# Kernel tuning notes

Measured on AMD Instinct MI355X. Metric: run time of the kernel, lower is better.

Reference implementation:

```python
import jax, jax.numpy as jnp
import numpy as np

GROUP_SIZE = 128

def setup_inputs() -> dict:
    key = jax.random.key(0)
    k0, k1, k2, k3 = jax.random.split(key, 4)
    B, S, K, N = 4, 16, 8192, 28672
    G = GROUP_SIZE
    x = jax.random.normal(k0, (B, S, K), dtype=jnp.float16)
    # packed uint8 stored as int32 (2 int4 nibbles per byte along K)
    w_packed = jax.random.randint(k1, (K // 2, N), 0, 256, dtype=jnp.int32)
    # per-group positive scales, typical magnitude for int4 quant of fp16 weights
    scales = (jax.random.uniform(k2, (K // G, N), dtype=jnp.float32) * 0.02 + 1e-4).astype(jnp.float16)
    bias = (jax.random.normal(k3, (N,), dtype=jnp.float16) * 0.02).astype(jnp.float16)
    return {"x": x, "w_packed": w_packed, "scales": scales, "bias": bias}

def _dequant(w_packed, scales):
    # w_packed: [K//2, N] ints in [0,256); low nibble -> even k, high nibble -> odd k
    low = (w_packed & 15) - 8          # [K//2, N] int32 in [-8, 7]
    high = ((w_packed >> 4) & 15) - 8  # [K//2, N]
    Kh, N = w_packed.shape
    w_int = jnp.stack([low, high], axis=1).reshape(Kh * 2, N)  # interleave -> [K, N]
    s = jnp.repeat(scales, GROUP_SIZE, axis=0)                 # [K, N] fp16
    return w_int.astype(jnp.float16) * s                       # [K, N] fp16

def reference(x, w_packed, scales, bias):
    # x: [B, S, K] fp16 -> y: [B, S, N] fp16
    w = _dequant(w_packed, scales)                 # [K, N] fp16
    lead = x.shape[:-1]
    x2 = x.reshape(-1, x.shape[-1])                # [M, K]
    # fp32 accumulation, fp16 output (matches Triton kernel's tl.dot accumulator)
    y = jnp.dot(x2, w, preferred_element_type=jnp.float32).astype(jnp.float16)
    y = y + bias
    return y.reshape(*lead, -1)
```

## Files before the change

### kernel.cpp

```cpp
#include <hip/hip_runtime.h>


typedef short  short8  __attribute__((ext_vector_type(8)));
typedef float  float4v __attribute__((ext_vector_type(4)));
typedef int    int4v   __attribute__((ext_vector_type(4)));
typedef unsigned int uint4v __attribute__((ext_vector_type(4)));

constexpr int Kd = 8192;
constexpr int Nd = 28672;
constexpr int KSPLIT = 4;
constexpr int GPS = 16;
constexpr int LDS_STRIDE = 68;

__device__ __forceinline__ unsigned f32_to_bf16_rn(float f) {
    unsigned u = __builtin_bit_cast(unsigned, f);
    return (u + 0x7FFFu + ((u >> 16) & 1u)) >> 16;
}

__global__ __launch_bounds__(256)
void init_y_kernel(const float* __restrict__ bias, float* __restrict__ y) {
    const int gid = blockIdx.x * 256 + threadIdx.x;
    const int m  = gid / (Nd / 4);
    const int nq = gid % (Nd / 4);
    ((float4v*)y)[(long)m * (Nd / 4) + nq] = ((const float4v*)bias)[nq];
}

__global__ __launch_bounds__(256)
void cvt_x_kernel(const float* __restrict__ x, unsigned short* __restrict__ o) {
    const int i = (blockIdx.x * 256 + threadIdx.x) * 8;
    float4v a = *(const float4v*)(x + i);
    float4v b = *(const float4v*)(x + i + 4);
    union { unsigned short s[8]; short8 v; } r;
    #pragma unroll
    for (int j = 0; j < 4; ++j) {
        r.s[j]     = (unsigned short)f32_to_bf16_rn(a[j]);
        r.s[4 + j] = (unsigned short)f32_to_bf16_rn(b[j]);
    }
    *(short8*)(o + i) = r.v;
}

__global__ __launch_bounds__(256, 6)
void int4_main_kernel(const unsigned short* __restrict__ xb,
                      const int*            __restrict__ wp,
                      const float*          __restrict__ scales,
                      float*                __restrict__ y)
{
    __shared__ unsigned lds_w[64 * LDS_STRIDE];

    const int t    = threadIdx.x;
    const int lane = t & 63;
    const int wv   = t >> 6;
    const int q    = lane >> 4;
    const int c    = lane & 15;
    const int n0   = blockIdx.x * 64;
    const int kz   = blockIdx.y;

    const int sr = t >> 4, ss = t & 15;
    const int*   wp_b = wp + (long)(kz * 1024 + sr) * Nd + n0 + 4 * ss;
    const float* sc_b = scales + (long)(kz * GPS) * Nd + n0 + 4 * ss;

    const unsigned short* xb_b = xb + (long)c * Kd + kz * 2048 + q * 8;

    float4v acc[4] = {};

    for (int g = 0; g < GPS; ++g) {
        const float4v s4 = *(const float4v*)(sc_b + (long)g * Nd);
        const int* wg = wp_b + (long)g * 64 * Nd;
        #pragma unroll
        for (int i = 0; i < 4; ++i) {
            int4v v = *(const int4v*)(wg + (long)i * 16 * Nd);
            uint4v pk;
            #pragma unroll
            for (int j = 0; j < 4; ++j) {
                float lo = (float)((v[j] & 15) - 8) * s4[j];
                float hi = (float)(((v[j] >> 4) & 15) - 8) * s4[j];
                pk[j] = f32_to_bf16_rn(lo) | (f32_to_bf16_rn(hi) << 16);
            }
            *(uint4v*)&lds_w[(i * 16 + sr) * LDS_STRIDE + 4 * ss] = pk;
        }
        __syncthreads();

        const unsigned short* xg = xb_b + g * 128;
        #pragma unroll
        for (int it = 0; it < 4; ++it) {
            union { short8 h; unsigned u[4]; } bu;
            #pragma unroll
            for (int i = 0; i < 4; ++i)
                bu.u[i] = lds_w[(it * 16 + q * 4 + i) * LDS_STRIDE + wv * 16 + c];
            const short8 b = bu.h;

            const unsigned short* xk = xg + it * 32;
            #pragma unroll
            for (int mt = 0; mt < 4; ++mt) {
                short8 a = *(const short8*)(xk + (long)mt * 16 * Kd);
                acc[mt] = __builtin_amdgcn_mfma_f32_16x16x32_bf16(a, b, acc[mt], 0, 0, 0);
            }
        }
        __syncthreads();
    }

    const int nw = n0 + wv * 16 + c;
    #pragma unroll
    for (int mt = 0; mt < 4; ++mt)
        #pragma unroll
        for (int r = 0; r < 4; ++r)
            atomicAdd(&y[(long)(mt * 16 + q * 4 + r) * Nd + nw], acc[mt][r]);
}

__global__ __launch_bounds__(256, 6)
void int4_main_nows_kernel(const float* __restrict__ xf,
                           const int*   __restrict__ wp,
                           const float* __restrict__ scales,
                           float*       __restrict__ y)
{
    __shared__ unsigned lds_w[64 * LDS_STRIDE];
    const int t = threadIdx.x, lane = t & 63, wv = t >> 6;
    const int q = lane >> 4, c = lane & 15;
    const int n0 = blockIdx.x * 64, kz = blockIdx.y;
    const int sr = t >> 4, ss = t & 15;
    const int*   wp_b = wp + (long)(kz * 1024 + sr) * Nd + n0 + 4 * ss;
    const float* sc_b = scales + (long)(kz * GPS) * Nd + n0 + 4 * ss;
    const float* xf_b = xf + (long)c * Kd + kz * 2048 + q * 8;
    float4v acc[4] = {};

    for (int g = 0; g < GPS; ++g) {
        const float4v s4 = *(const float4v*)(sc_b + (long)g * Nd);
        const int* wg = wp_b + (long)g * 64 * Nd;
        #pragma unroll
        for (int i = 0; i < 4; ++i) {
            int4v v = *(const int4v*)(wg + (long)i * 16 * Nd);
            uint4v pk;
            #pragma unroll
            for (int j = 0; j < 4; ++j) {
                float lo = (float)((v[j] & 15) - 8) * s4[j];
                float hi = (float)(((v[j] >> 4) & 15) - 8) * s4[j];
                pk[j] = f32_to_bf16_rn(lo) | (f32_to_bf16_rn(hi) << 16);
            }
            *(uint4v*)&lds_w[(i * 16 + sr) * LDS_STRIDE + 4 * ss] = pk;
        }
        __syncthreads();
        const float* xg = xf_b + g * 128;
        #pragma unroll
        for (int it = 0; it < 4; ++it) {
            union { short8 h; unsigned u[4]; } bu;
            #pragma unroll
            for (int i = 0; i < 4; ++i)
                bu.u[i] = lds_w[(it * 16 + q * 4 + i) * LDS_STRIDE + wv * 16 + c];
            const short8 b = bu.h;
            const float* xk = xg + it * 32;
            #pragma unroll
            for (int mt = 0; mt < 4; ++mt) {
                float4v a0 = *(const float4v*)(xk + (long)mt * 16 * Kd);
                float4v a1 = *(const float4v*)(xk + (long)mt * 16 * Kd + 4);
                union { unsigned short s[8]; short8 v; } r;
                #pragma unroll
                for (int j = 0; j < 4; ++j) {
                    r.s[j]     = (unsigned short)f32_to_bf16_rn(a0[j]);
                    r.s[4 + j] = (unsigned short)f32_to_bf16_rn(a1[j]);
                }
                acc[mt] = __builtin_amdgcn_mfma_f32_16x16x32_bf16(r.v, b, acc[mt], 0, 0, 0);
            }
        }
        __syncthreads();
    }
    const int nw = n0 + wv * 16 + c;
    #pragma unroll
    for (int mt = 0; mt < 4; ++mt)
        #pragma unroll
        for (int r = 0; r < 4; ++r)
            atomicAdd(&y[(long)(mt * 16 + q * 4 + r) * Nd + nw], acc[mt][r]);
}

extern "C" void kernel_launch(void* const* d_in, const int* in_sizes, int n_in,
                              void* d_out, int out_size, void* d_ws, size_t ws_size,
                              hipStream_t stream) {
    const float* x      = (const float*)d_in[0];
    const int*   wp     = (const int*)d_in[1];
    const float* scales = (const float*)d_in[2];
    const float* bias   = (const float*)d_in[3];
    float*       y      = (float*)d_out;

    init_y_kernel<<<dim3(1792), dim3(256), 0, stream>>>(bias, y);

    const size_t xb_bytes = (size_t)64 * Kd * sizeof(unsigned short);
    dim3 grid(Nd / 64, KSPLIT);
    dim3 block(256);

    if (ws_size >= xb_bytes) {
        unsigned short* xb = (unsigned short*)d_ws;
        cvt_x_kernel<<<dim3(256), dim3(256), 0, stream>>>(x, xb);
        int4_main_kernel<<<grid, block, 0, stream>>>(xb, wp, scales, y);
    } else {
        int4_main_nows_kernel<<<grid, block, 0, stream>>>(x, wp, scales, y);
    }
}
```

Before: 767.8 us.

## Double-buffer LDS and prefetch next weight group into registers

The main kernel now prefetches the next group's packed weights and scales into registers while the current group is dequantized and multiplied. It double-buffers the LDS tile so the trailing barrier can be dropped, and hoists all activation loads for the group ahead of the MFMA loop. Occupancy is lowered from 6 to 4 blocks per SM to leave room for the extra registers. The goal is to hide global-memory latency on the weight stream, at the cost of higher register pressure and fewer resident waves.

```diff
diff --git a/kernel.cpp b/kernel.cpp
--- a/kernel.cpp
+++ b/kernel.cpp
@@ -15,6 +15,10 @@
 __device__ __forceinline__ unsigned f32_to_bf16_rn(float f) {
     unsigned u = __builtin_bit_cast(unsigned, f);
     return (u + 0x7FFFu + ((u >> 16) & 1u)) >> 16;
+}
+
+__device__ __forceinline__ void sync_lds() {
+    asm volatile("s_waitcnt lgkmcnt(0)\n\ts_barrier" ::: "memory");
 }
 
 __global__ __launch_bounds__(256)
@@ -39,13 +43,13 @@
     *(short8*)(o + i) = r.v;
 }
 
-__global__ __launch_bounds__(256, 6)
+__global__ __launch_bounds__(256, 4)
 void int4_main_kernel(const unsigned short* __restrict__ xb,
                       const int*            __restrict__ wp,
                       const float*          __restrict__ scales,
                       float*                __restrict__ y)
 {
-    __shared__ unsigned lds_w[64 * LDS_STRIDE];
+    __shared__ unsigned lds_w[2 * 64 * LDS_STRIDE];
 
     const int t    = threadIdx.x;
     const int lane = t & 63;
@@ -58,45 +62,66 @@
     const int sr = t >> 4, ss = t & 15;
     const int*   wp_b = wp + (long)(kz * 1024 + sr) * Nd + n0 + 4 * ss;
     const float* sc_b = scales + (long)(kz * GPS) * Nd + n0 + 4 * ss;
-
     const unsigned short* xb_b = xb + (long)c * Kd + kz * 2048 + q * 8;
 
     float4v acc[4] = {};
+    int4v wc[4], wn[4];
+    float4v scur, snxt;
+
+    #pragma unroll
+    for (int i = 0; i < 4; ++i)
+        wc[i] = *(const int4v*)(wp_b + (long)i * 16 * Nd);
+    scur = *(const float4v*)(sc_b);
 
     for (int g = 0; g < GPS; ++g) {
-        const float4v s4 = *(const float4v*)(sc_b + (long)g * Nd);
-        const int* wg = wp_b + (long)g * 64 * Nd;
+        unsigned* buf = &lds_w[(g & 1) * (64 * LDS_STRIDE)];
+
+        const unsigned short* xg = xb_b + g * 128;
+        short8 areg[16];
+        #pragma unroll
+        for (int it = 0; it < 4; ++it)
+            #pragma unroll
+            for (int mt = 0; mt < 4; ++mt)
+                areg[it * 4 + mt] = *(const short8*)(xg + it * 32 + (long)mt * 16 * Kd);
+
+        if (g + 1 < GPS) {
+            const int* wg = wp_b + (long)(g + 1) * 64 * Nd;
+            #pragma unroll
+            for (int i = 0; i < 4; ++i)
+                wn[i] = *(const int4v*)(wg + (long)i * 16 * Nd);
+            snxt = *(const float4v*)(sc_b + (long)(g + 1) * Nd);
+        }
+
         #pragma unroll
         for (int i = 0; i < 4; ++i) {
-            int4v v = *(const int4v*)(wg + (long)i * 16 * Nd);
             uint4v pk;
             #pragma unroll
             for (int j = 0; j < 4; ++j) {
-                float lo = (float)((v[j] & 15) - 8) * s4[j];
-                float hi = (float)(((v[j] >> 4) & 15) - 8) * s4[j];
+                float lo = (float)((wc[i][j] & 15) - 8) * scur[j];
+                float hi = (float)(((wc[i][j] >> 4) & 15) - 8) * scur[j];
                 pk[j] = f32_to_bf16_rn(lo) | (f32_to_bf16_rn(hi) << 16);
             }
-            *(uint4v*)&lds_w[(i * 16 + sr) * LDS_STRIDE + 4 * ss] = pk;
-        }
-        __syncthreads();
-
-        const unsigned short* xg = xb_b + g * 128;
+            *(uint4v*)&buf[(i * 16 + sr) * LDS_STRIDE + 4 * ss] = pk;
+        }
+
+        sync_lds();
+
         #pragma unroll
         for (int it = 0; it < 4; ++it) {
             union { short8 h; unsigned u[4]; } bu;
             #pragma unroll
             for (int i = 0; i < 4; ++i)
-                bu.u[i] = lds_w[(it * 16 + q * 4 + i) * LDS_STRIDE + wv * 16 + c];
+                bu.u[i] = buf[(it * 16 + q * 4 + i) * LDS_STRIDE + wv * 16 + c];
             const short8 b = bu.h;
-
-            const unsigned short* xk = xg + it * 32;
-            #pragma unroll
-            for (int mt = 0; mt < 4; ++mt) {
-                short8 a = *(const short8*)(xk + (long)mt * 16 * Kd);
-                acc[mt] = __builtin_amdgcn_mfma_f32_16x16x32_bf16(a, b, acc[mt], 0, 0, 0);
-            }
-        }
-        __syncthreads();
+            #pragma unroll
+            for (int mt = 0; mt < 4; ++mt)
+                acc[mt] = __builtin_amdgcn_mfma_f32_16x16x32_bf16(
+                              areg[it * 4 + mt], b, acc[mt], 0, 0, 0);
+        }
+
+        #pragma unroll
+        for (int i = 0; i < 4; ++i) wc[i] = wn[i];
+        scur = snxt;
     }
 
     const int nw = n0 + wv * 16 + c;
```

New measurement: 755.1 us. Within noise of the previous version (-1.6%).

## Double-buffer weights and activations via async global-to-LDS loads with dequant at MFMA

Applied to the files above, without the earlier changes.

Rewrites the main int4 GEMV kernel to stream packed weights, bf16 activations and scales into LDS with global_load_lds async copies, double-buffered across half-groups with manual waitcnt/barrier sequencing. Dequantization now happens when B fragments are read from LDS, using an fma with a precomputed -8*scale, and both LDS tiles use XOR swizzles to avoid bank conflicts. The goal is to overlap HBM weight streaming with compute and to drop the register round trip of the old load-dequant-store loop. In exchange it uses more LDS, lowers the occupancy hint to 4, and relies on hand-written waitcnt counts being correct.

```diff
diff --git a/kernel.cpp b/kernel.cpp
--- a/kernel.cpp
+++ b/kernel.cpp
@@ -9,12 +9,16 @@
 constexpr int Kd = 8192;
 constexpr int Nd = 28672;
 constexpr int KSPLIT = 4;
-constexpr int GPS = 16;
-constexpr int LDS_STRIDE = 68;
 
 __device__ __forceinline__ unsigned f32_to_bf16_rn(float f) {
     unsigned u = __builtin_bit_cast(unsigned, f);
     return (u + 0x7FFFu + ((u >> 16) & 1u)) >> 16;
+}
+
+__device__ __forceinline__ void async16(const void* g, void* l) {
+    __builtin_amdgcn_global_load_lds(
+        (const __attribute__((address_space(1))) unsigned*)g,
+        (__attribute__((address_space(3))) unsigned*)l, 16, 0, 0);
 }
 
 __global__ __launch_bounds__(256)
@@ -39,64 +43,94 @@
     *(short8*)(o + i) = r.v;
 }
 
-__global__ __launch_bounds__(256, 6)
-void int4_main_kernel(const unsigned short* __restrict__ xb,
+__global__ __launch_bounds__(256, 4)
+void int4_main_kernel(const unsigned short* __restrict__ xw,
                       const int*            __restrict__ wp,
                       const float*          __restrict__ scales,
                       float*                __restrict__ y)
 {
-    __shared__ unsigned lds_w[64 * LDS_STRIDE];
-
-    const int t    = threadIdx.x;
-    const int lane = t & 63;
-    const int wv   = t >> 6;
-    const int q    = lane >> 4;
-    const int c    = lane & 15;
-    const int n0   = blockIdx.x * 64;
-    const int kz   = blockIdx.y;
-
-    const int sr = t >> 4, ss = t & 15;
-    const int*   wp_b = wp + (long)(kz * 1024 + sr) * Nd + n0 + 4 * ss;
-    const float* sc_b = scales + (long)(kz * GPS) * Nd + n0 + 4 * ss;
-
-    const unsigned short* xb_b = xb + (long)c * Kd + kz * 2048 + q * 8;
+    __shared__ unsigned wb0[2048], wb1[2048];
+    __shared__ unsigned xb0[2048], xb1[2048];
+    __shared__ unsigned sb[1024];
+
+    const int t = threadIdx.x, lane = t & 63, wv = t >> 6;
+    const int q = lane >> 4, c = lane & 15;
+    const int l4 = lane >> 4, l15 = lane & 15;
+    const int n0 = blockIdx.x * 64, kz = blockIdx.y;
+
+    const int* wsrc0; const int* wsrc1;
+    {
+        int r0 = wv * 8 + 0 * 4 + l4, c0 = (l15 * 4) ^ (((wv * 2 + 0) & 3) << 4);
+        int r1 = wv * 8 + 1 * 4 + l4, c1 = (l15 * 4) ^ (((wv * 2 + 1) & 3) << 4);
+        wsrc0 = wp + (long)(kz * 1024 + r0) * Nd + n0 + c0;
+        wsrc1 = wp + (long)(kz * 1024 + r1) * Nd + n0 + c1;
+    }
+    const unsigned short* xsrc0; const unsigned short* xsrc1;
+    {
+        int s0 = wv * 128 + 0 * 64 + lane, m0 = s0 >> 3, k0 = (s0 & 7) ^ (m0 & 7);
+        int s1 = wv * 128 + 1 * 64 + lane, m1 = s1 >> 3, k1 = (s1 & 7) ^ (m1 & 7);
+        xsrc0 = xw + (long)m0 * Kd + kz * 2048 + k0 * 8;
+        xsrc1 = xw + (long)m1 * Kd + kz * 2048 + k1 * 8;
+    }
+    const int ldof = wv * 512;
+
+    {
+        const float* ssrc = scales + (long)(kz * 16 + (t >> 4)) * Nd + n0 + (t & 15) * 4;
+        async16(ssrc, sb + wv * 256);
+    }
+    async16(wsrc0, wb0 + ldof);
+    async16(wsrc1, wb0 + ldof + 256);
+    async16(xsrc0, xb0 + ldof);
+    async16(xsrc1, xb0 + ldof + 256);
 
     float4v acc[4] = {};
 
-    for (int g = 0; g < GPS; ++g) {
-        const float4v s4 = *(const float4v*)(sc_b + (long)g * Nd);
-        const int* wg = wp_b + (long)g * 64 * Nd;
-        #pragma unroll
-        for (int i = 0; i < 4; ++i) {
-            int4v v = *(const int4v*)(wg + (long)i * 16 * Nd);
-            uint4v pk;
-            #pragma unroll
-            for (int j = 0; j < 4; ++j) {
-                float lo = (float)((v[j] & 15) - 8) * s4[j];
-                float hi = (float)(((v[j] >> 4) & 15) - 8) * s4[j];
-                pk[j] = f32_to_bf16_rn(lo) | (f32_to_bf16_rn(hi) << 16);
-            }
-            *(uint4v*)&lds_w[(i * 16 + sr) * LDS_STRIDE + 4 * ss] = pk;
-        }
-        __syncthreads();
-
-        const unsigned short* xg = xb_b + g * 128;
-        #pragma unroll
-        for (int it = 0; it < 4; ++it) {
+    auto stage = [&](int hg, unsigned* wbuf, unsigned* xbuf) {
+        const long wof = (long)hg * 32 * Nd;
+        const long xof = (long)hg * 64;
+        async16(wsrc0 + wof, wbuf + ldof);
+        async16(wsrc1 + wof, wbuf + ldof + 256);
+        async16(xsrc0 + xof, xbuf + ldof);
+        async16(xsrc1 + xof, xbuf + ldof + 256);
+    };
+
+    auto compute = [&](const unsigned* wbuf, const unsigned* xbuf, int g) {
+        const float s   = __builtin_bit_cast(float, sb[g * 64 + wv * 16 + c]);
+        const float m8s = -8.0f * s;
+        #pragma unroll
+        for (int it = 0; it < 2; ++it) {
             union { short8 h; unsigned u[4]; } bu;
             #pragma unroll
-            for (int i = 0; i < 4; ++i)
-                bu.u[i] = lds_w[(it * 16 + q * 4 + i) * LDS_STRIDE + wv * 16 + c];
-            const short8 b = bu.h;
-
-            const unsigned short* xk = xg + it * 32;
+            for (int i = 0; i < 4; ++i) {
+                unsigned v = wbuf[(it * 16 + q * 4 + i) * 64 + ((wv * 16 + c) ^ (q << 4))];
+                float lo = fmaf((float)(v & 15u), s, m8s);
+                float hi = fmaf((float)((v >> 4) & 15u), s, m8s);
+                bu.u[i] = f32_to_bf16_rn(lo) | (f32_to_bf16_rn(hi) << 16);
+            }
             #pragma unroll
             for (int mt = 0; mt < 4; ++mt) {
-                short8 a = *(const short8*)(xk + (long)mt * 16 * Kd);
-                acc[mt] = __builtin_amdgcn_mfma_f32_16x16x32_bf16(a, b, acc[mt], 0, 0, 0);
-            }
-        }
-        __syncthreads();
+                int m = mt * 16 + c;
+                int slot = m * 8 + ((it * 4 + q) ^ (c & 7));
+                short8 a = *(const short8*)(xbuf + slot * 4);
+                acc[mt] = __builtin_amdgcn_mfma_f32_16x16x32_bf16(a, bu.h, acc[mt], 0, 0, 0);
+            }
+        }
+    };
+
+    for (int hgp = 0; hgp < 16; ++hgp) {
+        const int hg = 2 * hgp;
+        stage(hg + 1, wb1, xb1);
+        asm volatile("s_waitcnt vmcnt(4)\ns_barrier" ::: "memory");
+        compute(wb0, xb0, hgp);
+        asm volatile("s_waitcnt lgkmcnt(0)\ns_barrier" ::: "memory");
+        if (hgp < 15) {
+            stage(hg + 2, wb0, xb0);
+            asm volatile("s_waitcnt vmcnt(4)\ns_barrier" ::: "memory");
+        } else {
+            asm volatile("s_waitcnt vmcnt(0)\ns_barrier" ::: "memory");
+        }
+        compute(wb1, xb1, hgp);
+        asm volatile("s_waitcnt lgkmcnt(0)\ns_barrier" ::: "memory");
     }
 
     const int nw = n0 + wv * 16 + c;
@@ -113,17 +147,18 @@
                            const float* __restrict__ scales,
                            float*       __restrict__ y)
 {
+    constexpr int LDS_STRIDE = 68;
     __shared__ unsigned lds_w[64 * LDS_STRIDE];
     const int t = threadIdx.x, lane = t & 63, wv = t >> 6;
     const int q = lane >> 4, c = lane & 15;
     const int n0 = blockIdx.x * 64, kz = blockIdx.y;
     const int sr = t >> 4, ss = t & 15;
     const int*   wp_b = wp + (long)(kz * 1024 + sr) * Nd + n0 + 4 * ss;
-    const float* sc_b = scales + (long)(kz * GPS) * Nd + n0 + 4 * ss;
+    const float* sc_b = scales + (long)(kz * 16) * Nd + n0 + 4 * ss;
     const float* xf_b = xf + (long)c * Kd + kz * 2048 + q * 8;
     float4v acc[4] = {};
 
-    for (int g = 0; g < GPS; ++g) {
+    for (int g = 0; g < 16; ++g) {
         const float4v s4 = *(const float4v*)(sc_b + (long)g * Nd);
         const int* wg = wp_b + (long)g * 64 * Nd;
         #pragma unroll
```

Result: faster. 630.7 us (-17.9%).
